# Optimization experiments

Measured on AMD Instinct MI355X. Metric: run time of the kernel, lower is better.

## Reference

```python
import jax, jax.numpy as jnp
import numpy as np

L, B, D = 2048, 8, 1024


def setup_inputs() -> dict:
    key = jax.random.key(0)
    ks = jax.random.split(key, 10)
    s = 0.02  # Linear weight scale to keep exp(k) in a sane range
    return {
        "x": jax.random.normal(ks[0], (L, B, D), jnp.float32),
        "mu_k": jax.random.uniform(ks[1], (D,), jnp.float32),
        "mu_v": jax.random.uniform(ks[2], (D,), jnp.float32),
        "mu_r": jax.random.uniform(ks[3], (D,), jnp.float32),
        "Wk": jax.random.normal(ks[4], (D, D), jnp.float32) * s,
        "Wv": jax.random.normal(ks[5], (D, D), jnp.float32) * s,
        "Wr": jax.random.normal(ks[6], (D, D), jnp.float32) * s,
        "W_out": jax.random.normal(ks[7], (D, D), jnp.float32) * s,
        "w": jax.random.uniform(ks[8], (D,), jnp.float32),
        "u": jax.random.uniform(ks[9], (D,), jnp.float32),
    }


def reference(x, mu_k, mu_v, mu_r, Wk, Wv, Wr, W_out, w, u):
    # x: [L, B, D] (time-first). Fresh hidden state => numerator/denominator_last = 0.
    Lx = x.shape[0]
    # PreviousMixing (RWKV token shift): mu*x_t + (1-mu)*x_{t-1}, zero initial prev.
    x_prev = jnp.concatenate([jnp.zeros_like(x[:1]), x[:-1]], axis=0)
    k = (mu_k * x + (1.0 - mu_k) * x_prev) @ Wk.T
    v = (mu_v * x + (1.0 - mu_v) * x_prev) @ Wv.T
    r = (mu_r * x + (1.0 - mu_r) * x_prev) @ Wr.T

    w_neg = -jnp.exp(w)                      # [D], negative decay
    exp_w = jnp.exp(w_neg)                   # [D]
    t = jnp.arange(Lx, dtype=x.dtype)
    ewp = jnp.exp(w_neg[None, :] * t[:, None])  # [L, D] decay progression

    exp_k = jnp.exp(k)                       # [L, B, D]
    exp_k_v = exp_k * v

    n = 2 * Lx  # zero-padded FFT length for linear convolution
    f_ewp = jnp.fft.rfft(ewp, n=n, axis=0)[:, None, :]        # [n/2+1, 1, D]
    f_ek = jnp.fft.rfft(exp_k, n=n, axis=0)                   # [n/2+1, B, D]
    f_ekv = jnp.fft.rfft(exp_k_v, n=n, axis=0)
    conv_ek = jnp.fft.irfft(f_ewp * f_ek, axis=0)[:Lx]         # [L, B, D]
    conv_ekv = jnp.fft.irfft(f_ewp * f_ekv, axis=0)[:Lx]

    # Initial numerator_last/denominator_last are zeros, so their terms vanish.
    denominator = conv_ek
    numerator = conv_ekv

    exp_u = jnp.exp(u)
    denominator_out = (denominator - exp_k) / exp_w + exp_k * exp_u
    numerator_out = (numerator - exp_k_v) / exp_w + exp_k_v * exp_u
    return (jax.nn.sigmoid(r) * numerator_out / denominator_out) @ W_out.T
```

## Files before the change

### kernel.cpp

```cpp
#include <hip/hip_runtime.h>
#include <cstddef>
#include <cstdint>

#define Lq 2048
#define Bq 8
#define Dq 1024
#define Mq (Lq*Bq)

typedef _Float16 f16;
typedef _Float16 f16x2 __attribute__((ext_vector_type(2)));
typedef _Float16 f16x8 __attribute__((ext_vector_type(8)));
typedef float f32x4 __attribute__((ext_vector_type(4)));

typedef const __attribute__((address_space(1))) uint32_t GU32;
typedef __attribute__((address_space(3))) uint32_t LU32;

#define BAR()    asm volatile("s_barrier" ::: "memory")
#define WAITV4() asm volatile("s_waitcnt vmcnt(4)" ::: "memory")

__global__ __launch_bounds__(256) void cvt3_k(const float* __restrict__ a,
                                              const float* __restrict__ b,
                                              const float* __restrict__ c,
                                              f16* __restrict__ dst) {
  int i = (blockIdx.x * 256 + threadIdx.x) * 8;
  const float* s = (blockIdx.y == 0) ? a : (blockIdx.y == 1) ? b : c;
  f16* d = dst + (size_t)blockIdx.y * ((size_t)Dq * Dq) + i;
  float4 v0 = *(const float4*)(s + i);
  float4 v1 = *(const float4*)(s + i + 4);
  f16x8 o;
  o[0] = (f16)v0.x; o[1] = (f16)v0.y; o[2] = (f16)v0.z; o[3] = (f16)v0.w;
  o[4] = (f16)v1.x; o[5] = (f16)v1.y; o[6] = (f16)v1.z; o[7] = (f16)v1.w;
  *(f16x8*)d = o;
}

__global__ __launch_bounds__(256) void cvt1_k(const float* __restrict__ s,
                                              f16* __restrict__ d) {
  int i = (blockIdx.x * 256 + threadIdx.x) * 8;
  float4 v0 = *(const float4*)(s + i);
  float4 v1 = *(const float4*)(s + i + 4);
  f16x8 o;
  o[0] = (f16)v0.x; o[1] = (f16)v0.y; o[2] = (f16)v0.z; o[3] = (f16)v0.w;
  o[4] = (f16)v1.x; o[5] = (f16)v1.y; o[6] = (f16)v1.z; o[7] = (f16)v1.w;
  *(f16x8*)(d + i) = o;
}

__global__ __launch_bounds__(256) void prep_k(const float* __restrict__ x,
                                              const float* __restrict__ muk,
                                              const float* __restrict__ muv,
                                              const float* __restrict__ mur,
                                              f16* __restrict__ xk,
                                              f16* __restrict__ xv,
                                              f16* __restrict__ xr) {
  size_t i = ((size_t)blockIdx.x * 256 + threadIdx.x) * 8;
  int col = (int)(i & (Dq - 1));
  float4 a0 = *(const float4*)(x + i);
  float4 a1 = *(const float4*)(x + i + 4);
  float4 p0 = make_float4(0.f, 0.f, 0.f, 0.f), p1 = p0;
  if (i >= (size_t)(Bq * Dq)) {
    p0 = *(const float4*)(x + i - Bq * Dq);
    p1 = *(const float4*)(x + i - Bq * Dq + 4);
  }
  float av[8] = {a0.x, a0.y, a0.z, a0.w, a1.x, a1.y, a1.z, a1.w};
  float pv[8] = {p0.x, p0.y, p0.z, p0.w, p1.x, p1.y, p1.z, p1.w};

#define MIX8(MU, DST)                                                          \
  {                                                                            \
    float4 m0 = *(const float4*)((MU) + col);                                  \
    float4 m1 = *(const float4*)((MU) + col + 4);                              \
    float mv8[8] = {m0.x, m0.y, m0.z, m0.w, m1.x, m1.y, m1.z, m1.w};           \
    f16x8 o;                                                                   \
    _Pragma("unroll")                                                          \
    for (int j = 0; j < 8; ++j) o[j] = (f16)(pv[j] + mv8[j] * (av[j] - pv[j]));\
    *(f16x8*)((DST) + i) = o;                                                  \
  }
  MIX8(muk, xk)
  MIX8(muv, xv)
  MIX8(mur, xr)
#undef MIX8
}

template<int OUTF32>
__global__ __launch_bounds__(512, 2) void gemm8p_k(const f16* __restrict__ A,
                                                   const f16* __restrict__ W,
                                                   void* __restrict__ Cv) {
  __shared__ f16 lds[2][2][256][64];
  const int tid  = threadIdx.x;
  const int lane = tid & 63;
  const int wid  = tid >> 6;
  const int wr   = wid >> 2;
  const int wc   = wid & 3;
  const int wg = (blockIdx.x & 7) * 32 + (blockIdx.x >> 3);
  const int bx = wg & 3;
  const int by = wg >> 2;

  const int fr = lane & 15;
  const int fg = lane >> 4;
  const int c0 = ((fg    ) ^ (fr & 7)) * 8;
  const int c1 = ((fg ^ 4) ^ (fr & 7)) * 8;

  const int rowoff = wid * 8 + (lane >> 3);
  const int scol   = ((lane & 7) ^ (lane >> 3)) * 8;
  const f16* Ab = A + (size_t)(by * 256) * Dq;
  const f16* Wb = W + (size_t)(bx * 256) * Dq;

#define STAGE(bufi, op, h, base, kt) do {                                      \
    const f16* _g = (base) + (size_t)((h) * 128 + rowoff) * Dq + (kt) * 64 + scol; \
    __builtin_amdgcn_global_load_lds((GU32*)_g,                                \
        (LU32*)&lds[bufi][op][(h) * 128 + wid * 8][0], 16, 0, 0);              \
    __builtin_amdgcn_global_load_lds((GU32*)(_g + (size_t)64 * Dq),            \
        (LU32*)&lds[bufi][op][(h) * 128 + 64 + wid * 8][0], 16, 0, 0);         \
  } while (0)

  f16x8 af[4][2], bf0[2][2], bf1[2][2];
  f32x4 acc[8][4] = {};

#define LOAD_A(bufi, mh)                                                       \
  _Pragma("unroll")                                                            \
  for (int mi2 = 0; mi2 < 4; ++mi2) {                                          \
    af[mi2][0] = *(const f16x8*)&lds[bufi][0][wr * 128 + (mh) * 64 + mi2 * 16 + fr][c0]; \
    af[mi2][1] = *(const f16x8*)&lds[bufi][0][wr * 128 + (mh) * 64 + mi2 * 16 + fr][c1]; \
  }
#define LOAD_B(bufi, nh, bf)                                                   \
  _Pragma("unroll")                                                            \
  for (int ni2 = 0; ni2 < 2; ++ni2) {                                          \
    bf[ni2][0] = *(const f16x8*)&lds[bufi][1][wc * 64 + (nh) * 32 + ni2 * 16 + fr][c0]; \
    bf[ni2][1] = *(const f16x8*)&lds[bufi][1][wc * 64 + (nh) * 32 + ni2 * 16 + fr][c1]; \
  }
#define MFMA_Q(mh, nh, bf)                                                     \
  __builtin_amdgcn_s_setprio(1);                                               \
  _Pragma("unroll")                                                            \
  for (int ks = 0; ks < 2; ++ks)                                               \
    _Pragma("unroll")                                                          \
    for (int mi2 = 0; mi2 < 4; ++mi2)                                          \
      _Pragma("unroll")                                                        \
      for (int ni2 = 0; ni2 < 2; ++ni2)                                        \
        acc[(mh) * 4 + mi2][(nh) * 2 + ni2] =                                  \
            __builtin_amdgcn_mfma_f32_16x16x32_f16(af[mi2][ks], bf[ni2][ks],   \
                acc[(mh) * 4 + mi2][(nh) * 2 + ni2], 0, 0, 0);                 \
  __builtin_amdgcn_s_setprio(0);

  STAGE(0, 0, 0, Ab, 0); STAGE(0, 0, 1, Ab, 0);
  STAGE(0, 1, 0, Wb, 0); STAGE(0, 1, 1, Wb, 0);
  STAGE(1, 1, 0, Wb, 1); STAGE(1, 1, 1, Wb, 1);
  WAITV4();
  BAR();

  for (int i = 0; i < 8; ++i) {
    const int t1 = 2 * i + 1;
    int t2 = 2 * i + 2; if (t2 > 15) t2 = 15;
    int t3 = 2 * i + 3; if (t3 > 15) t3 = 15;
    LOAD_A(0, 0); LOAD_B(0, 0, bf0);
    STAGE(1, 0, 0, Ab, t1);
    BAR(); MFMA_Q(0, 0, bf0); BAR();
    LOAD_B(0, 1, bf1);
    STAGE(1, 0, 1, Ab, t1);
    BAR(); MFMA_Q(0, 1, bf1); BAR();
    LOAD_A(0, 1);
    STAGE(0, 1, 0, Wb, t2);
    BAR(); MFMA_Q(1, 1, bf1); BAR();
    STAGE(0, 1, 1, Wb, t2);
    BAR(); MFMA_Q(1, 0, bf0); WAITV4(); BAR();
    LOAD_A(1, 0); LOAD_B(1, 0, bf0);
    STAGE(0, 0, 0, Ab, t2);
    BAR(); MFMA_Q(0, 0, bf0); BAR();
    LOAD_B(1, 1, bf1);
    STAGE(0, 0, 1, Ab, t2);
    BAR(); MFMA_Q(0, 1, bf1); BAR();
    LOAD_A(1, 1);
    STAGE(1, 1, 0, Wb, t3);
    BAR(); MFMA_Q(1, 1, bf1); BAR();
    STAGE(1, 1, 1, Wb, t3);
    BAR(); MFMA_Q(1, 0, bf0); WAITV4(); BAR();
  }

#pragma unroll
  for (int mi = 0; mi < 8; ++mi) {
    const int row0 = by * 256 + wr * 128 + mi * 16 + fg * 4;
#pragma unroll
    for (int ni = 0; ni < 4; ++ni) {
      const int col = bx * 256 + wc * 64 + ni * 16 + fr;
      if (OUTF32) {
        float* C = (float*)Cv;
#pragma unroll
        for (int j = 0; j < 4; ++j)
          C[(size_t)(row0 + j) * Dq + col] = acc[mi][ni][j];
      } else {
        f16* C = (f16*)Cv;
#pragma unroll
        for (int j = 0; j < 4; ++j)
          C[(size_t)(row0 + j) * Dq + col] = (f16)acc[mi][ni][j];
      }
    }
  }
#undef STAGE
#undef LOAD_A
#undef LOAD_B
#undef MFMA_Q
}

constexpr int CHUNK = 32, LOOKBACK = 16;

__global__ __launch_bounds__(256) void scan_k(const f16* __restrict__ kk,
                                              const f16* __restrict__ vv,
                                              const f16* rr,
                                              const float* __restrict__ w,
                                              const float* __restrict__ u,
                                              f16* y) {
  const int unit = blockIdx.y * 256 + threadIdx.x;
  const int d = (unit & 511) * 2;
  const int b = unit >> 9;
  const int t0 = blockIdx.x * CHUNK;

  const float dec0 = __expf(-__expf(w[d]));
  const float dec1 = __expf(-__expf(w[d + 1]));
  const float eu0  = __expf(u[d]);
  const float eu1  = __expf(u[d + 1]);

  float A0 = 0.f, A1 = 0.f, Av0 = 0.f, Av1 = 0.f;
  const size_t base = (size_t)b * Dq + d;

  if (t0 > 0) {
#pragma unroll 4
    for (int t = t0 - LOOKBACK; t < t0; ++t) {
      size_t idx = (size_t)t * (Bq * Dq) + base;
      f16x2 k2 = *(const f16x2*)(kk + idx);
      f16x2 v2 = *(const f16x2*)(vv + idx);
      float ek0 = __expf((float)k2[0]), ek1 = __expf((float)k2[1]);
      A0  = fmaf(dec0, A0,  ek0);
      A1  = fmaf(dec1, A1,  ek1);
      Av0 = fmaf(dec0, Av0, ek0 * (float)v2[0]);
      Av1 = fmaf(dec1, Av1, ek1 * (float)v2[1]);
    }
  }
#pragma unroll 4
  for (int t = t0; t < t0 + CHUNK; ++t) {
    size_t idx = (size_t)t * (Bq * Dq) + base;
    f16x2 k2 = *(const f16x2*)(kk + idx);
    f16x2 v2 = *(const f16x2*)(vv + idx);
    f16x2 r2 = *(const f16x2*)(rr + idx);
    float ek0 = __expf((float)k2[0]), ek1 = __expf((float)k2[1]);
    float ekv0 = ek0 * (float)v2[0], ekv1 = ek1 * (float)v2[1];
    float den0 = fmaf(ek0,  eu0, A0),  den1 = fmaf(ek1,  eu1, A1);
    float num0 = fmaf(ekv0, eu0, Av0), num1 = fmaf(ekv1, eu1, Av1);
    float s0 = __builtin_amdgcn_rcpf(1.f + __expf(-(float)r2[0]));
    float s1 = __builtin_amdgcn_rcpf(1.f + __expf(-(float)r2[1]));
    f16x2 o;
    o[0] = (f16)(s0 * num0 * __builtin_amdgcn_rcpf(den0));
    o[1] = (f16)(s1 * num1 * __builtin_amdgcn_rcpf(den1));
    *(f16x2*)(y + idx) = o;
    A0  = fmaf(dec0, A0,  ek0);
    A1  = fmaf(dec1, A1,  ek1);
    Av0 = fmaf(dec0, Av0, ekv0);
    Av1 = fmaf(dec1, Av1, ekv1);
  }
}

extern "C" void kernel_launch(void* const* d_in, const int* in_sizes, int n_in,
                              void* d_out, int out_size, void* d_ws, size_t ws_size,
                              hipStream_t stream) {
  const float* x    = (const float*)d_in[0];
  const float* mu_k = (const float*)d_in[1];
  const float* mu_v = (const float*)d_in[2];
  const float* mu_r = (const float*)d_in[3];
  const float* Wk   = (const float*)d_in[4];
  const float* Wv   = (const float*)d_in[5];
  const float* Wr   = (const float*)d_in[6];
  const float* Wo   = (const float*)d_in[7];
  const float* w    = (const float*)d_in[8];
  const float* u    = (const float*)d_in[9];

  f16* xk = (f16*)d_ws;
  f16* xv = xk + (size_t)Mq * Dq;
  f16* xr = xv + (size_t)Mq * Dq;
  f16* kb = xr + (size_t)Mq * Dq;
  f16* vb = kb + (size_t)Mq * Dq;
  f16* rb = vb + (size_t)Mq * Dq;
  f16* w16  = (f16*)d_out;
  f16* wo16 = xk;

  cvt3_k<<<dim3(512, 3), 256, 0, stream>>>(Wk, Wv, Wr, w16);
  prep_k<<<8192, 256, 0, stream>>>(x, mu_k, mu_v, mu_r, xk, xv, xr);
  gemm8p_k<0><<<256, 512, 0, stream>>>(xk, w16,                       kb);
  cvt1_k<<<512, 256, 0, stream>>>(Wo, wo16);
  gemm8p_k<0><<<256, 512, 0, stream>>>(xv, w16 + (size_t)Dq * Dq,     vb);
  gemm8p_k<0><<<256, 512, 0, stream>>>(xr, w16 + 2 * (size_t)Dq * Dq, rb);
  scan_k<<<dim3(Lq / CHUNK, 16), 256, 0, stream>>>(kb, vb, rb, w, u, rb);
  gemm8p_k<1><<<256, 512, 0, stream>>>(rb, wo16, (float*)d_out);
}
```

Baseline: 216.4 us.

## Batch three projection GEMMs into one launch and coarsen prep kernel

Merges the k, v and r projection GEMMs into a single 768-block launch that selects its operands by block index. The weight conversion is reordered so r's weights come first. The mixing prep kernel now handles four row groups per thread with the mu vectors loaded once, and the scan loops are fully unrolled. The aim is to cut launch overhead and tail underutilization from three 256-block GEMMs on a large GPU, at the cost of more register pressure in the unrolled loops.

Result: no change. 218.2 us (+0.8%).

```diff
diff --git a/kernel.cpp b/kernel.cpp
--- a/kernel.cpp
+++ b/kernel.cpp
@@ -51,47 +51,53 @@
                                               f16* __restrict__ xk,
                                               f16* __restrict__ xv,
                                               f16* __restrict__ xr) {
-  size_t i = ((size_t)blockIdx.x * 256 + threadIdx.x) * 8;
-  int col = (int)(i & (Dq - 1));
-  float4 a0 = *(const float4*)(x + i);
-  float4 a1 = *(const float4*)(x + i + 4);
-  float4 p0 = make_float4(0.f, 0.f, 0.f, 0.f), p1 = p0;
-  if (i >= (size_t)(Bq * Dq)) {
-    p0 = *(const float4*)(x + i - Bq * Dq);
-    p1 = *(const float4*)(x + i - Bq * Dq + 4);
-  }
-  float av[8] = {a0.x, a0.y, a0.z, a0.w, a1.x, a1.y, a1.z, a1.w};
-  float pv[8] = {p0.x, p0.y, p0.z, p0.w, p1.x, p1.y, p1.z, p1.w};
-
-#define MIX8(MU, DST)                                                          \
-  {                                                                            \
-    float4 m0 = *(const float4*)((MU) + col);                                  \
+  const size_t base0 = ((size_t)blockIdx.x * 256 + threadIdx.x) * 8;
+  const int col = (int)(base0 & (Dq - 1));
+
+  float mk[8], mv[8], mr[8];
+#define LD8(MU, DST)                                                           \
+  { float4 m0 = *(const float4*)((MU) + col);                                  \
     float4 m1 = *(const float4*)((MU) + col + 4);                              \
-    float mv8[8] = {m0.x, m0.y, m0.z, m0.w, m1.x, m1.y, m1.z, m1.w};           \
-    f16x8 o;                                                                   \
-    _Pragma("unroll")                                                          \
-    for (int j = 0; j < 8; ++j) o[j] = (f16)(pv[j] + mv8[j] * (av[j] - pv[j]));\
-    *(f16x8*)((DST) + i) = o;                                                  \
-  }
-  MIX8(muk, xk)
-  MIX8(muv, xv)
-  MIX8(mur, xr)
+    DST[0]=m0.x; DST[1]=m0.y; DST[2]=m0.z; DST[3]=m0.w;                        \
+    DST[4]=m1.x; DST[5]=m1.y; DST[6]=m1.z; DST[7]=m1.w; }
+  LD8(muk, mk) LD8(muv, mv) LD8(mur, mr)
+#undef LD8
+
+#pragma unroll
+  for (int it = 0; it < 4; ++it) {
+    size_t i = base0 + (size_t)it * (8u * 524288u);
+    float4 a0 = *(const float4*)(x + i);
+    float4 a1 = *(const float4*)(x + i + 4);
+    float4 p0 = make_float4(0.f, 0.f, 0.f, 0.f), p1 = p0;
+    if (i >= (size_t)(Bq * Dq)) {
+      p0 = *(const float4*)(x + i - Bq * Dq);
+      p1 = *(const float4*)(x + i - Bq * Dq + 4);
+    }
+    float av[8] = {a0.x, a0.y, a0.z, a0.w, a1.x, a1.y, a1.z, a1.w};
+    float pv[8] = {p0.x, p0.y, p0.z, p0.w, p1.x, p1.y, p1.z, p1.w};
+#define MIX8(MV, DST)                                                          \
+    { f16x8 o;                                                                 \
+      _Pragma("unroll")                                                        \
+      for (int j = 0; j < 8; ++j) o[j] = (f16)(pv[j] + MV[j] * (av[j] - pv[j]));\
+      *(f16x8*)((DST) + i) = o; }
+    MIX8(mk, xk)
+    MIX8(mv, xv)
+    MIX8(mr, xr)
 #undef MIX8
+  }
 }
 
 template<int OUTF32>
-__global__ __launch_bounds__(512, 2) void gemm8p_k(const f16* __restrict__ A,
-                                                   const f16* __restrict__ W,
-                                                   void* __restrict__ Cv) {
+__device__ __forceinline__ void gemm_core(const f16* __restrict__ A,
+                                          const f16* __restrict__ W,
+                                          void* __restrict__ Cv,
+                                          int bx, int by) {
   __shared__ f16 lds[2][2][256][64];
   const int tid  = threadIdx.x;
   const int lane = tid & 63;
   const int wid  = tid >> 6;
   const int wr   = wid >> 2;
   const int wc   = wid & 3;
-  const int wg = (blockIdx.x & 7) * 32 + (blockIdx.x >> 3);
-  const int bx = wg & 3;
-  const int by = wg >> 2;
 
   const int fr = lane & 15;
   const int fg = lane >> 4;
@@ -198,6 +204,29 @@
 #undef MFMA_Q
 }
 
+__global__ __launch_bounds__(512, 2) void gemm3_k(const f16* __restrict__ xr,
+                                                  const f16* __restrict__ xv,
+                                                  const f16* __restrict__ xk,
+                                                  const f16* __restrict__ w16,
+                                                  f16* __restrict__ rb,
+                                                  f16* __restrict__ vb,
+                                                  f16* __restrict__ kb) {
+  const int s = blockIdx.x >> 8;
+  const int inner = blockIdx.x & 255;
+  const int wg = (inner & 7) * 32 + (inner >> 3);
+  const f16* A = (s == 0) ? xr : (s == 1) ? xv : xk;
+  const f16* W = w16 + (size_t)s * Dq * Dq;
+  f16* C = (s == 0) ? rb : (s == 1) ? vb : kb;
+  gemm_core<0>(A, W, C, wg & 3, wg >> 2);
+}
+
+__global__ __launch_bounds__(512, 2) void gemmO_k(const f16* __restrict__ A,
+                                                  const f16* __restrict__ W,
+                                                  float* __restrict__ C) {
+  const int wg = (blockIdx.x & 7) * 32 + (blockIdx.x >> 3);
+  gemm_core<1>(A, W, C, wg & 3, wg >> 2);
+}
+
 constexpr int CHUNK = 32, LOOKBACK = 16;
 
 __global__ __launch_bounds__(256) void scan_k(const f16* __restrict__ kk,
@@ -220,7 +249,7 @@
   const size_t base = (size_t)b * Dq + d;
 
   if (t0 > 0) {
-#pragma unroll 4
+#pragma unroll
     for (int t = t0 - LOOKBACK; t < t0; ++t) {
       size_t idx = (size_t)t * (Bq * Dq) + base;
       f16x2 k2 = *(const f16x2*)(kk + idx);
@@ -232,7 +261,7 @@
       Av1 = fmaf(dec1, Av1, ek1 * (float)v2[1]);
     }
   }
-#pragma unroll 4
+#pragma unroll
   for (int t = t0; t < t0 + CHUNK; ++t) {
     size_t idx = (size_t)t * (Bq * Dq) + base;
     f16x2 k2 = *(const f16x2*)(kk + idx);
@@ -278,12 +307,10 @@
   f16* w16  = (f16*)d_out;
   f16* wo16 = xk;
 
-  cvt3_k<<<dim3(512, 3), 256, 0, stream>>>(Wk, Wv, Wr, w16);
-  prep_k<<<8192, 256, 0, stream>>>(x, mu_k, mu_v, mu_r, xk, xv, xr);
-  gemm8p_k<0><<<256, 512, 0, stream>>>(xk, w16,                       kb);
+  cvt3_k<<<dim3(512, 3), 256, 0, stream>>>(Wr, Wv, Wk, w16);
+  prep_k<<<2048, 256, 0, stream>>>(x, mu_k, mu_v, mu_r, xk, xv, xr);
+  gemm3_k<<<768, 512, 0, stream>>>(xr, xv, xk, w16, rb, vb, kb);
   cvt1_k<<<512, 256, 0, stream>>>(Wo, wo16);
-  gemm8p_k<0><<<256, 512, 0, stream>>>(xv, w16 + (size_t)Dq * Dq,     vb);
-  gemm8p_k<0><<<256, 512, 0, stream>>>(xr, w16 + 2 * (size_t)Dq * Dq, rb);
   scan_k<<<dim3(Lq / CHUNK, 16), 256, 0, stream>>>(kb, vb, rb, w, u, rb);
-  gemm8p_k<1><<<256, 512, 0, stream>>>(rb, wo16, (float*)d_out);
-}
+  gemmO_k<<<256, 512, 0, stream>>>(rb, wo16, (float*)d_out);
+}
```
